# Performance work log

Hardware: AMD Instinct MI355X
Metric: run time of the kernel (lower is better)

## Reference

```python
import jax, jax.numpy as jnp
import numpy as np

N_NODES = 50000
N_EDGES = 800000
NFEAT, NHID, NCLASS = 512, 256, 64


def spmm(src, dst, w, h):
    """Sparse adj @ dense h via gather + segment_sum.
    out[i] = sum over edges e with dst[e]==i of w[e] * h[src[e]]."""
    msgs = h[src] * w[:, None]  # [E, d]
    return jax.ops.segment_sum(msgs, dst, num_segments=N_NODES)


def setup_inputs() -> dict:
    key = jax.random.key(0)
    ks = jax.random.split(key, 10)
    return {
        "x": jax.random.normal(ks[0], (N_NODES, NFEAT), dtype=jnp.float32),
        "edge_src0": jax.random.randint(ks[1], (N_EDGES,), 0, N_NODES),
        "edge_dst0": jax.random.randint(ks[2], (N_EDGES,), 0, N_NODES),
        "edge_w0": jax.random.uniform(ks[3], (N_EDGES,), dtype=jnp.float32),
        "edge_src1": jax.random.randint(ks[4], (N_EDGES,), 0, N_NODES),
        "edge_dst1": jax.random.randint(ks[5], (N_EDGES,), 0, N_NODES),
        "edge_w1": jax.random.uniform(ks[6], (N_EDGES,), dtype=jnp.float32),
        "W1": jax.random.normal(ks[7], (NFEAT, NHID), dtype=jnp.float32) * (1.0 / np.sqrt(NFEAT)),
        "b1": jnp.zeros((NHID,), dtype=jnp.float32),
        "W2": jax.random.normal(ks[8], (NHID, NCLASS), dtype=jnp.float32) * (1.0 / np.sqrt(NHID)),
        "b2": jnp.zeros((NCLASS,), dtype=jnp.float32),
    }


def reference(x, edge_src0, edge_dst0, edge_w0, edge_src1, edge_dst1, edge_w1, W1, b1, W2, b2):
    # Layer 1: GCN conv (skip=False) + ReLU. Dropout is identity in eval mode.
    h = jax.nn.relu(spmm(edge_src0, edge_dst0, edge_w0, x @ W1) + b1)
    # Layer 2: GCN conv (skip=False)
    logits = spmm(edge_src1, edge_dst1, edge_w1, h @ W2) + b2
    return jax.nn.log_softmax(logits, axis=1)
```

## Files before the change

kernel.cpp:

```cpp
#include <hip/hip_runtime.h>

#define N_NODES 50000
#define N_EDGES 800000
#define NFEAT   512
#define NHID    256
#define NCLASS  64

#define MTILES     ((N_NODES + 63) / 64)

#define NBUCK      196
#define BCAP       5632
#define BIN_CHUNK  4096
#define BIN_BLOCKS ((N_EDGES + BIN_CHUNK - 1) / BIN_CHUNK)

typedef short short8  __attribute__((ext_vector_type(8)));
typedef float floatx4 __attribute__((ext_vector_type(4)));
typedef float floatx2 __attribute__((ext_vector_type(2)));

__device__ inline short f2bf(float f) {
    unsigned u = __builtin_bit_cast(unsigned, f);
    u += 0x7FFF + ((u >> 16) & 1);
    return (short)(u >> 16);
}
__device__ inline float bf2f(short v) {
    unsigned u = ((unsigned)(unsigned short)v) << 16;
    return __builtin_bit_cast(float, u);
}
__device__ inline int pack_edge(int src, float w) {
    return (src & 0xFFFF) | ((int)(unsigned short)f2bf(w) << 16);
}

#if defined(__has_builtin)
#if __has_builtin(__builtin_amdgcn_cvt_pk_f32_fp8) && __has_builtin(__builtin_amdgcn_cvt_pk_fp8_f32)
#define HAVE_HW_FP8 1
#endif
#endif

__device__ inline unsigned char f2fp8(float f) {
#ifdef HAVE_HW_FP8
    return (unsigned char)(__builtin_amdgcn_cvt_pk_fp8_f32(f, f, 0, false) & 0xFF);
#else
    unsigned u = __builtin_bit_cast(unsigned, f);
    unsigned s = (u >> 31) << 7;
    float af = fabsf(f);
    if (!(af >= 0.0009765625f)) {
        int q = (int)(af * 512.f + 0.5f);
        if (q > 7) q = 7;
        return (unsigned char)(s | q);
    }
    if (af > 448.f) return (unsigned char)(s | 0x7E);
    int ex; float mf = frexpf(af, &ex);
    int E = ex - 1;
    if (E < -6) {
        int q = (int)(af * 512.f + 0.5f);
        if (q > 7) q = 7;
        return (unsigned char)(s | q);
    }
    int m = (int)((2.f * mf - 1.f) * 8.f + 0.5f);
    if (m == 8) { m = 0; ++E; }
    if (E > 8) return (unsigned char)(s | 0x7E);
    return (unsigned char)(s | ((E + 7) << 3) | m);
#endif
}

__device__ inline void fp8x8_to_f32(uint2 v, float* o) {
#ifdef HAVE_HW_FP8
    floatx2 f0 = __builtin_amdgcn_cvt_pk_f32_fp8((int)v.x, false);
    floatx2 f1 = __builtin_amdgcn_cvt_pk_f32_fp8((int)v.x, true);
    floatx2 f2 = __builtin_amdgcn_cvt_pk_f32_fp8((int)v.y, false);
    floatx2 f3 = __builtin_amdgcn_cvt_pk_f32_fp8((int)v.y, true);
    o[0] = f0[0]; o[1] = f0[1]; o[2] = f1[0]; o[3] = f1[1];
    o[4] = f2[0]; o[5] = f2[1]; o[6] = f3[0]; o[7] = f3[1];
#else
    unsigned w[2] = {v.x, v.y};
    #pragma unroll
    for (int k = 0; k < 8; ++k) {
        unsigned char b = (w[k >> 2] >> ((k & 3) * 8)) & 0xFF;
        int sg = b >> 7, e = (b >> 3) & 15, m = b & 7;
        float val = e ? ldexpf(1.f + m * 0.125f, e - 7) : ldexpf(m * 0.125f, -6);
        o[k] = sg ? -val : val;
    }
#endif
}

typedef __attribute__((address_space(3))) void       lds_void;
typedef __attribute__((address_space(1))) const void glb_void;
__device__ inline void gload_lds16(const void* g, void* l) {
    __builtin_amdgcn_global_load_lds((glb_void*)g, (lds_void*)l, 16, 0, 0);
}

__global__ __launch_bounds__(256) void cast_w1t_kernel(const float* __restrict__ W1,
                                                       short* __restrict__ Wt) {
    __shared__ short tile[64][72];
    const int t  = threadIdx.x;
    const int k0 = (blockIdx.x >> 2) << 6;
    const int n0 = (blockIdx.x & 3) << 6;
    {
        int kr = t >> 2, ng = (t & 3) << 4;
        const float* src = W1 + (size_t)(k0 + kr) * NHID + n0 + ng;
        float4 v0 = ((const float4*)src)[0], v1 = ((const float4*)src)[1];
        float4 v2 = ((const float4*)src)[2], v3 = ((const float4*)src)[3];
        short* d = &tile[kr][ng];
        d[0]=f2bf(v0.x); d[1]=f2bf(v0.y); d[2]=f2bf(v0.z); d[3]=f2bf(v0.w);
        d[4]=f2bf(v1.x); d[5]=f2bf(v1.y); d[6]=f2bf(v1.z); d[7]=f2bf(v1.w);
        d[8]=f2bf(v2.x); d[9]=f2bf(v2.y); d[10]=f2bf(v2.z); d[11]=f2bf(v2.w);
        d[12]=f2bf(v3.x); d[13]=f2bf(v3.y); d[14]=f2bf(v3.z); d[15]=f2bf(v3.w);
    }
    __syncthreads();
    {
        int nr = t >> 2, kg = (t & 3) << 4;
        short8 o0, o1;
        #pragma unroll
        for (int j = 0; j < 8; ++j) { o0[j] = tile[kg + j][nr]; o1[j] = tile[kg + 8 + j][nr]; }
        short* d = Wt + (size_t)(n0 + nr) * NFEAT + k0 + kg;
        *(short8*)d = o0;
        *(short8*)(d + 8) = o1;
    }
}

__global__ __launch_bounds__(256) void cast_w2t_kernel(const float* __restrict__ W2,
                                                       short* __restrict__ W2t) {
    __shared__ short tile[64][72];
    const int t  = threadIdx.x;
    const int k0 = blockIdx.x << 6;
    {
        int kr = t >> 2, ng = (t & 3) << 4;
        const float* src = W2 + (size_t)(k0 + kr) * NCLASS + ng;
        float4 v0 = ((const float4*)src)[0], v1 = ((const float4*)src)[1];
        float4 v2 = ((const float4*)src)[2], v3 = ((const float4*)src)[3];
        short* d = &tile[kr][ng];
        d[0]=f2bf(v0.x); d[1]=f2bf(v0.y); d[2]=f2bf(v0.z); d[3]=f2bf(v0.w);
        d[4]=f2bf(v1.x); d[5]=f2bf(v1.y); d[6]=f2bf(v1.z); d[7]=f2bf(v1.w);
        d[8]=f2bf(v2.x); d[9]=f2bf(v2.y); d[10]=f2bf(v2.z); d[11]=f2bf(v2.w);
        d[12]=f2bf(v3.x); d[13]=f2bf(v3.y); d[14]=f2bf(v3.z); d[15]=f2bf(v3.w);
    }
    __syncthreads();
    {
        int nr = t >> 2, kg = (t & 3) << 4;
        short8 o0, o1;
        #pragma unroll
        for (int j = 0; j < 8; ++j) { o0[j] = tile[kg + j][nr]; o1[j] = tile[kg + 8 + j][nr]; }
        short* d = W2t + (size_t)nr * NHID + k0 + kg;
        *(short8*)d = o0;
        *(short8*)(d + 8) = o1;
    }
}

__global__ __launch_bounds__(256) void binscatter_kernel(
    const int* __restrict__ es0, const int* __restrict__ ed0, const float* __restrict__ ew0,
    int* __restrict__ cur0, int2* __restrict__ bin0,
    const int* __restrict__ es1, const int* __restrict__ ed1, const float* __restrict__ ew1,
    int* __restrict__ cur1, int2* __restrict__ bin1) {
    __shared__ int hist[NBUCK];
    const int list = blockIdx.x >= BIN_BLOCKS;
    const int cb   = blockIdx.x - list * BIN_BLOCKS;
    const int*   es  = list ? es1 : es0;
    const int*   ed  = list ? ed1 : ed0;
    const float* ew  = list ? ew1 : ew0;
    int*         cur = list ? cur1 : cur0;
    int2*        bin = list ? bin1 : bin0;

    const int e0 = cb * BIN_CHUNK;
    const int e1 = min(e0 + BIN_CHUNK, N_EDGES);
    const int t  = threadIdx.x;

    if (t < NBUCK) hist[t] = 0;
    __syncthreads();
    for (int e = e0 + t; e < e1; e += 256)
        atomicAdd(&hist[ed[e] >> 8], 1);
    __syncthreads();
    if (t < NBUCK) hist[t] = atomicAdd(&cur[t], hist[t]);
    __syncthreads();
    for (int e = e0 + t; e < e1; e += 256) {
        int d = ed[e];
        int b = d >> 8;
        int p = atomicAdd(&hist[b], 1);
        if (p < BCAP) {
            int2 v; v.x = pack_edge(es[e], ew[e]); v.y = d;
            bin[(size_t)b * BCAP + p] = v;
        }
    }
}

__global__ __launch_bounds__(256) void bucket_scan_kernel(const int* __restrict__ cur0, int* __restrict__ bb0,
                                                          const int* __restrict__ cur1, int* __restrict__ bb1) {
    __shared__ int s[256];
    const int* cur = blockIdx.x ? cur1 : cur0;
    int*       bb  = blockIdx.x ? bb1  : bb0;
    int t = threadIdx.x;
    int v = (t < NBUCK) ? min(cur[t], BCAP) : 0;
    s[t] = v;
    __syncthreads();
    for (int off = 1; off < 256; off <<= 1) {
        int a = (t >= off) ? s[t - off] : 0;
        __syncthreads();
        s[t] += a;
        __syncthreads();
    }
    if (t < NBUCK) bb[t] = s[t] - v;
}

__global__ __launch_bounds__(256) void bucket_csr_kernel(
    const int* __restrict__ cur0, const int* __restrict__ bb0, const int2* __restrict__ bin0,
    int* __restrict__ deg0, int* __restrict__ base0, int* __restrict__ edge0,
    const int* __restrict__ cur1, const int* __restrict__ bb1, const int2* __restrict__ bin1,
    int* __restrict__ deg1, int* __restrict__ base1, int* __restrict__ edge1) {
    __shared__ int dh[256];
    __shared__ int sc[256];
    const int list = blockIdx.x >= NBUCK;
    const int b    = blockIdx.x - list * NBUCK;
    const int*  cur  = list ? cur1  : cur0;
    const int*  bb   = list ? bb1   : bb0;
    const int2* bin  = (list ? bin1 : bin0) + (size_t)b * BCAP;
    int*        deg  = list ? deg1  : deg0;
    int*        base = list ? base1 : base0;
    int*        edge = list ? edge1 : edge0;

    const int len   = min(cur[b], BCAP);
    const int gbase = bb[b];
    const int n0    = b << 8;
    const int t     = threadIdx.x;

    dh[t] = 0;
    __syncthreads();
    for (int i = t; i < len; i += 256)
        atomicAdd(&dh[bin[i].y & 255], 1);
    __syncthreads();
    int v = dh[t];
    sc[t] = v;
    __syncthreads();
    for (int off = 1; off < 256; off <<= 1) {
        int a = (t >= off) ? sc[t - off] : 0;
        __syncthreads();
        sc[t] += a;
        __syncthreads();
    }
    int excl = sc[t] - v;
    int node = n0 + t;
    if (node < N_NODES) { deg[node] = v; base[node] = gbase + excl; }
    dh[t] = gbase + excl;
    __syncthreads();
    for (int i = t; i < len; i += 256) {
        int2 ev = bin[i];
        int p = atomicAdd(&dh[ev.y & 255], 1);
        edge[p] = ev.x;
    }
}

__global__ __launch_bounds__(256) void gemm1_mfma_kernel(const float* __restrict__ x,
                                                         const short* __restrict__ Wt,
                                                         unsigned char* __restrict__ h0f) {
    __shared__ short As[64 * 64];
    __shared__ short Bs[256 * 64];
    const int tid  = threadIdx.x;
    const int wave = tid >> 6, lane = tid & 63;
    const int mlo  = lane & 15, q = lane >> 4;
    const int m0   = blockIdx.x * 64;

    const int ar = tid >> 2;
    const int cp = (tid & 3) * 2;
    int arow = m0 + ar; if (arow >= N_NODES) arow = N_NODES - 1;
    const float* aptr = x + (size_t)arow * NFEAT + cp * 8;

    const int brl = lane >> 3;
    const int bsl = lane & 7;

    floatx4 acc[4][4] = {};

    for (int kc = 0; kc < NFEAT; kc += 64) {
        #pragma unroll
        for (int i = 0; i < 8; ++i) {
            int r  = wave * 64 + i * 8 + brl;
            int sc2 = bsl ^ (r & 7);
            gload_lds16(Wt + (size_t)r * NFEAT + kc + sc2 * 8,
                        &Bs[(wave * 64 + i * 8) * 64]);
        }
        float4 a0 = *(const float4*)(aptr + kc);
        float4 a1 = *(const float4*)(aptr + kc + 4);
        float4 a2 = *(const float4*)(aptr + kc + 8);
        float4 a3 = *(const float4*)(aptr + kc + 12);
        short8 p0, p1;
        p0[0]=f2bf(a0.x); p0[1]=f2bf(a0.y); p0[2]=f2bf(a0.z); p0[3]=f2bf(a0.w);
        p0[4]=f2bf(a1.x); p0[5]=f2bf(a1.y); p0[6]=f2bf(a1.z); p0[7]=f2bf(a1.w);
        p1[0]=f2bf(a2.x); p1[1]=f2bf(a2.y); p1[2]=f2bf(a2.z); p1[3]=f2bf(a2.w);
        p1[4]=f2bf(a3.x); p1[5]=f2bf(a3.y); p1[6]=f2bf(a3.z); p1[7]=f2bf(a3.w);
        *(short8*)&As[ar * 64 + ((cp     ) ^ (ar & 7)) * 8] = p0;
        *(short8*)&As[ar * 64 + ((cp + 1) ^ (ar & 7)) * 8] = p1;
        __syncthreads();

        #pragma unroll
        for (int h = 0; h < 2; ++h) {
            short8 afv[4], bfv[4];
            #pragma unroll
            for (int t = 0; t < 4; ++t) {
                int r = t * 16 + mlo;
                afv[t] = *(const short8*)&As[r * 64 + ((h * 4 + q) ^ (r & 7)) * 8];
            }
            #pragma unroll
            for (int u = 0; u < 4; ++u) {
                int r = wave * 64 + u * 16 + mlo;
                bfv[u] = *(const short8*)&Bs[r * 64 + ((h * 4 + q) ^ (r & 7)) * 8];
            }
            #pragma unroll
            for (int t = 0; t < 4; ++t)
                #pragma unroll
                for (int u = 0; u < 4; ++u)
                    acc[t][u] = __builtin_amdgcn_mfma_f32_16x16x32_bf16(afv[t], bfv[u], acc[t][u], 0, 0, 0);
        }
        __syncthreads();
    }

    #pragma unroll
    for (int t = 0; t < 4; ++t) {
        #pragma unroll
        for (int r = 0; r < 4; ++r) {
            int row = m0 + t * 16 + q * 4 + r;
            if (row < N_NODES) {
                #pragma unroll
                for (int u = 0; u < 4; ++u)
                    h0f[(size_t)row * NHID + wave * 64 + u * 16 + mlo] = f2fp8(acc[t][u][r]);
            }
        }
    }
}

__global__ __launch_bounds__(256) void spmm1_pull_kernel(const int* __restrict__ base,
                                                         const int* __restrict__ deg,
                                                         const int* __restrict__ edge_s,
                                                         const unsigned char* __restrict__ h0f,
                                                         short* __restrict__ agg0b) {
    const int node = blockIdx.x * 4 + (threadIdx.x >> 6);
    const int lane = threadIdx.x & 63;
    const int slot = lane >> 5;
    const int c    = lane & 31;
    const int start = base[node];
    const int len   = deg[node];

    float acc[8] = {0.f,0.f,0.f,0.f,0.f,0.f,0.f,0.f};

    int eA = 0, eB = 0, eC = 0, eD = 0;
    uint2 z = {0u, 0u};
    uint2 hA = z, hB = z, hC = z;
    if (slot     < len) eA = edge_s[start + slot];
    if (slot + 2 < len) eB = edge_s[start + slot + 2];
    if (slot + 4 < len) eC = edge_s[start + slot + 4];
    if (slot + 6 < len) eD = edge_s[start + slot + 6];
    if (slot     < len) hA = *(const uint2*)(h0f + (size_t)(eA & 0xFFFF) * NHID + c * 8);
    if (slot + 2 < len) hB = *(const uint2*)(h0f + (size_t)(eB & 0xFFFF) * NHID + c * 8);
    if (slot + 4 < len) hC = *(const uint2*)(h0f + (size_t)(eC & 0xFFFF) * NHID + c * 8);

    int jr = slot + 6;
    int je = slot + 8;
    for (int j = slot; j < len; j += 2) {
        float wt = bf2f((short)((unsigned)eA >> 16));
        float f[8];
        fp8x8_to_f32(hA, f);
        #pragma unroll
        for (int k = 0; k < 8; ++k) acc[k] += wt * f[k];
        eA = eB; hA = hB;
        eB = eC; hB = hC;
        eC = eD;
        if (jr < len) hC = *(const uint2*)(h0f + (size_t)(eC & 0xFFFF) * NHID + c * 8);
        if (je < len) eD = edge_s[start + je];
        jr += 2; je += 2;
    }

    #pragma unroll
    for (int k = 0; k < 8; ++k) acc[k] += __shfl_xor(acc[k], 32);
    if (slot == 0) {
        short8 ob;
        #pragma unroll
        for (int k = 0; k < 8; ++k) ob[k] = f2bf(acc[k]);
        *(short8*)(agg0b + (size_t)node * NHID + c * 8) = ob;
    }
}

__global__ __launch_bounds__(256) void gemm2_mfma_kernel(const short* __restrict__ agg0b,
                                                         const float* __restrict__ b1,
                                                         const short* __restrict__ W2t,
                                                         short* __restrict__ h2b) {
    __shared__ short Bs[64 * 256];
    __shared__ short As[64 * 64];
    const int tid  = threadIdx.x;
    const int wave = tid >> 6, lane = tid & 63;
    const int mlo  = lane & 15, q = lane >> 4;
    const int m0   = blockIdx.x * 64;

    {
        int n = tid >> 2;
        #pragma unroll
        for (int j = 0; j < 8; ++j) {
            int c  = (tid & 3) * 8 + j;
            int s2 = c ^ (n & 7);
            *(short8*)&Bs[n * 256 + s2 * 8] =
                *(const short8*)(W2t + (size_t)n * NHID + c * 8);
        }
    }

    const int ar = tid >> 2;
    const int cp = (tid & 3) * 2;
    int arow = m0 + ar; if (arow >= N_NODES) arow = N_NODES - 1;
    const short* aptr = agg0b + (size_t)arow * NHID + cp * 8;

    floatx4 acc[4] = {};

    for (int kc = 0; kc < NHID; kc += 64) {
        short8 s0 = *(const short8*)(aptr + kc);
        short8 s1 = *(const short8*)(aptr + kc + 8);
        float4 c0 = *(const float4*)(b1 + kc + cp * 8);
        float4 c1 = *(const float4*)(b1 + kc + cp * 8 + 4);
        float4 c2 = *(const float4*)(b1 + kc + cp * 8 + 8);
        float4 c3 = *(const float4*)(b1 + kc + cp * 8 + 12);
        float v0 = bf2f(s0[0]) + c0.x, v1 = bf2f(s0[1]) + c0.y;
        float v2 = bf2f(s0[2]) + c0.z, v3 = bf2f(s0[3]) + c0.w;
        float v4 = bf2f(s0[4]) + c1.x, v5 = bf2f(s0[5]) + c1.y;
        float v6 = bf2f(s0[6]) + c1.z, v7 = bf2f(s0[7]) + c1.w;
        float v8 = bf2f(s1[0]) + c2.x, v9 = bf2f(s1[1]) + c2.y;
        float vA = bf2f(s1[2]) + c2.z, vB = bf2f(s1[3]) + c2.w;
        float vC = bf2f(s1[4]) + c3.x, vD = bf2f(s1[5]) + c3.y;
        float vE = bf2f(s1[6]) + c3.z, vF = bf2f(s1[7]) + c3.w;
        short8 p0, p1;
        p0[0]=f2bf(v0>0.f?v0:0.f); p0[1]=f2bf(v1>0.f?v1:0.f); p0[2]=f2bf(v2>0.f?v2:0.f); p0[3]=f2bf(v3>0.f?v3:0.f);
        p0[4]=f2bf(v4>0.f?v4:0.f); p0[5]=f2bf(v5>0.f?v5:0.f); p0[6]=f2bf(v6>0.f?v6:0.f); p0[7]=f2bf(v7>0.f?v7:0.f);
        p1[0]=f2bf(v8>0.f?v8:0.f); p1[1]=f2bf(v9>0.f?v9:0.f); p1[2]=f2bf(vA>0.f?vA:0.f); p1[3]=f2bf(vB>0.f?vB:0.f);
        p1[4]=f2bf(vC>0.f?vC:0.f); p1[5]=f2bf(vD>0.f?vD:0.f); p1[6]=f2bf(vE>0.f?vE:0.f); p1[7]=f2bf(vF>0.f?vF:0.f);
        *(short8*)&As[ar * 64 + ((cp     ) ^ (ar & 7)) * 8] = p0;
        *(short8*)&As[ar * 64 + ((cp + 1) ^ (ar & 7)) * 8] = p1;
        __syncthreads();

        short8 afv[2];
        {
            int r = wave * 16 + mlo;
            afv[0] = *(const short8*)&As[r * 64 + ((    q) ^ (r & 7)) * 8];
            afv[1] = *(const short8*)&As[r * 64 + ((4 + q) ^ (r & 7)) * 8];
        }
        #pragma unroll
        for (int u = 0; u < 4; ++u) {
            int r = u * 16 + mlo;
            #pragma unroll
            for (int h = 0; h < 2; ++h) {
                int ch = (kc >> 3) + h * 4 + q;
                short8 bv = *(const short8*)&Bs[r * 256 + (ch ^ (r & 7)) * 8];
                acc[u] = __builtin_amdgcn_mfma_f32_16x16x32_bf16(afv[h], bv, acc[u], 0, 0, 0);
            }
        }
        __syncthreads();
    }

    #pragma unroll
    for (int r = 0; r < 4; ++r) {
        int row = m0 + wave * 16 + q * 4 + r;
        if (row < N_NODES) {
            #pragma unroll
            for (int u = 0; u < 4; ++u)
                h2b[(size_t)row * NCLASS + u * 16 + mlo] = f2bf(acc[u][r]);
        }
    }
}

__global__ __launch_bounds__(256) void spmm2_lsm_kernel(const int* __restrict__ base,
                                                        const int* __restrict__ deg,
                                                        const int* __restrict__ edge_s,
                                                        const short* __restrict__ h2b,
                                                        const float* __restrict__ b2,
                                                        float* __restrict__ out) {
    const int node = blockIdx.x * 4 + (threadIdx.x >> 6);
    const int lane = threadIdx.x & 63;
    const int slot = lane >> 3;
    const int f    = lane & 7;
    const int start = base[node];
    const int len   = deg[node];

    float acc[8] = {0.f,0.f,0.f,0.f,0.f,0.f,0.f,0.f};
    int j = slot;
    int e = 0;
    short8 hv = {0,0,0,0,0,0,0,0};
    if (j < len) {
        e  = edge_s[start + j];
        hv = *(const short8*)(h2b + (size_t)(e & 0xFFFF) * NCLASS + f * 8);
    }
    while (j < len) {
        float wt = bf2f((short)((unsigned)e >> 16));
        int jn = j + 8;
        int en = e; short8 hn = hv;
        if (jn < len) {
            en = edge_s[start + jn];
            hn = *(const short8*)(h2b + (size_t)(en & 0xFFFF) * NCLASS + f * 8);
        }
        #pragma unroll
        for (int k = 0; k < 8; ++k) acc[k] += wt * bf2f(hv[k]);
        e = en; hv = hn; j = jn;
    }
    #pragma unroll
    for (int k = 0; k < 8; ++k) {
        acc[k] += __shfl_xor(acc[k], 8);
        acc[k] += __shfl_xor(acc[k], 16);
        acc[k] += __shfl_xor(acc[k], 32);
    }
    float4 c0 = *(const float4*)(b2 + f * 8);
    float4 c1 = *(const float4*)(b2 + f * 8 + 4);
    float v[8];
    v[0] = acc[0] + c0.x; v[1] = acc[1] + c0.y; v[2] = acc[2] + c0.z; v[3] = acc[3] + c0.w;
    v[4] = acc[4] + c1.x; v[5] = acc[5] + c1.y; v[6] = acc[6] + c1.z; v[7] = acc[7] + c1.w;
    float m = v[0];
    #pragma unroll
    for (int k = 1; k < 8; ++k) m = fmaxf(m, v[k]);
    m = fmaxf(m, __shfl_xor(m, 1));
    m = fmaxf(m, __shfl_xor(m, 2));
    m = fmaxf(m, __shfl_xor(m, 4));
    float s = 0.f;
    #pragma unroll
    for (int k = 0; k < 8; ++k) s += __expf(v[k] - m);
    s += __shfl_xor(s, 1);
    s += __shfl_xor(s, 2);
    s += __shfl_xor(s, 4);
    float ls = m + __logf(s);
    if (slot == 0) {
        float4 o0 = {v[0] - ls, v[1] - ls, v[2] - ls, v[3] - ls};
        float4 o1 = {v[4] - ls, v[5] - ls, v[6] - ls, v[7] - ls};
        float* p = out + (size_t)node * NCLASS + f * 8;
        *(float4*)p = o0;
        *(float4*)(p + 4) = o1;
    }
}

extern "C" void kernel_launch(void* const* d_in, const int* in_sizes, int n_in,
                              void* d_out, int out_size, void* d_ws, size_t ws_size,
                              hipStream_t stream) {
    const float* x   = (const float*)d_in[0];
    const int*   es0 = (const int*)  d_in[1];
    const int*   ed0 = (const int*)  d_in[2];
    const float* ew0 = (const float*)d_in[3];
    const int*   es1 = (const int*)  d_in[4];
    const int*   ed1 = (const int*)  d_in[5];
    const float* ew1 = (const float*)d_in[6];
    const float* W1  = (const float*)d_in[7];
    const float* b1  = (const float*)d_in[8];
    const float* W2  = (const float*)d_in[9];
    const float* b2  = (const float*)d_in[10];
    float* out = (float*)d_out;

    char* ws = (char*)d_ws;
    const size_t SZ_H0 = (size_t)N_NODES * NHID * sizeof(short);
    const size_t SZ_BIN = (size_t)NBUCK * BCAP * sizeof(int2);
    unsigned char* h0f = (unsigned char*)ws;
    short* h2b   = (short*)ws;
    short* agg0b = (short*)(ws + (size_t)N_NODES * NHID * sizeof(float));

    int2* bin0 = (int2*)(ws + SZ_H0);
    int2* bin1 = (int2*)(ws + SZ_H0 + SZ_BIN);

    char* c1 = ws + 44000000;
    int* deg1  = (int*)c1;
    int* base1 = deg1 + N_NODES;
    int* edge1 = base1 + N_NODES;
    int* cur0  = edge1 + N_EDGES;
    int* cur1  = cur0 + 256;
    int* bb0   = cur1 + 256;
    int* bb1   = bb0 + 256;

    int*   deg0  = (int*)d_out;
    int*   base0 = deg0 + N_NODES;
    int*   edge0 = base0 + N_NODES;
    short* Wt    = (short*)((char*)d_out + (8u << 20));
    short* W2t   = (short*)((char*)d_out + (9u << 20));

    hipMemsetAsync(cur0, 0, 512 * sizeof(int), stream);
    binscatter_kernel<<<2 * BIN_BLOCKS, 256, 0, stream>>>(es0, ed0, ew0, cur0, bin0,
                                                          es1, ed1, ew1, cur1, bin1);
    bucket_scan_kernel<<<2, 256, 0, stream>>>(cur0, bb0, cur1, bb1);
    bucket_csr_kernel<<<2 * NBUCK, 256, 0, stream>>>(cur0, bb0, bin0, deg0, base0, edge0,
                                                     cur1, bb1, bin1, deg1, base1, edge1);

    cast_w1t_kernel<<<32, 256, 0, stream>>>(W1, Wt);
    cast_w2t_kernel<<<4, 256, 0, stream>>>(W2, W2t);

    gemm1_mfma_kernel<<<MTILES, 256, 0, stream>>>(x, Wt, h0f);
    spmm1_pull_kernel<<<N_NODES / 4, 256, 0, stream>>>(base0, deg0, edge0, h0f, agg0b);

    gemm2_mfma_kernel<<<MTILES, 256, 0, stream>>>(agg0b, b1, W2t, h2b);
    spmm2_lsm_kernel<<<N_NODES / 4, 256, 0, stream>>>(base1, deg1, edge1, h2b, b2, out);
}
```

Baseline: 328.8 us.

## Merge prep kernels, fold bucket scan into CSR, double-buffer GEMM1, split SpMM1 features

Fuses edge binning and the two weight-transpose casts into one prep kernel, and folds the bucket prefix scan into the per-bucket CSR kernel, cutting the launch count. The first GEMM gets double-buffered LDS so the next K-chunk loads overlap the MFMA work, at the cost of twice the shared memory. The first SpMM now splits each node's 256 features across two blocks with four edge slots per wave instead of two, adding parallelism and memory-level concurrency. The cost is redundant edge-list reads and an extra shuffle reduction.

```diff
diff --git a/kernel.cpp b/kernel.cpp
--- a/kernel.cpp
+++ b/kernel.cpp
@@ -12,6 +12,7 @@
 #define BCAP       5632
 #define BIN_CHUNK  4096
 #define BIN_BLOCKS ((N_EDGES + BIN_CHUNK - 1) / BIN_CHUNK)
+#define PREP_BLOCKS (2 * BIN_BLOCKS + 32 + 4)
 
 typedef short short8  __attribute__((ext_vector_type(8)));
 typedef float floatx4 __attribute__((ext_vector_type(4)));
@@ -89,140 +90,131 @@
     __builtin_amdgcn_global_load_lds((glb_void*)g, (lds_void*)l, 16, 0, 0);
 }
 
-__global__ __launch_bounds__(256) void cast_w1t_kernel(const float* __restrict__ W1,
-                                                       short* __restrict__ Wt) {
-    __shared__ short tile[64][72];
-    const int t  = threadIdx.x;
-    const int k0 = (blockIdx.x >> 2) << 6;
-    const int n0 = (blockIdx.x & 3) << 6;
-    {
-        int kr = t >> 2, ng = (t & 3) << 4;
-        const float* src = W1 + (size_t)(k0 + kr) * NHID + n0 + ng;
-        float4 v0 = ((const float4*)src)[0], v1 = ((const float4*)src)[1];
-        float4 v2 = ((const float4*)src)[2], v3 = ((const float4*)src)[3];
-        short* d = &tile[kr][ng];
-        d[0]=f2bf(v0.x); d[1]=f2bf(v0.y); d[2]=f2bf(v0.z); d[3]=f2bf(v0.w);
-        d[4]=f2bf(v1.x); d[5]=f2bf(v1.y); d[6]=f2bf(v1.z); d[7]=f2bf(v1.w);
-        d[8]=f2bf(v2.x); d[9]=f2bf(v2.y); d[10]=f2bf(v2.z); d[11]=f2bf(v2.w);
-        d[12]=f2bf(v3.x); d[13]=f2bf(v3.y); d[14]=f2bf(v3.z); d[15]=f2bf(v3.w);
-    }
-    __syncthreads();
-    {
-        int nr = t >> 2, kg = (t & 3) << 4;
-        short8 o0, o1;
-        #pragma unroll
-        for (int j = 0; j < 8; ++j) { o0[j] = tile[kg + j][nr]; o1[j] = tile[kg + 8 + j][nr]; }
-        short* d = Wt + (size_t)(n0 + nr) * NFEAT + k0 + kg;
-        *(short8*)d = o0;
-        *(short8*)(d + 8) = o1;
-    }
-}
-
-__global__ __launch_bounds__(256) void cast_w2t_kernel(const float* __restrict__ W2,
-                                                       short* __restrict__ W2t) {
-    __shared__ short tile[64][72];
-    const int t  = threadIdx.x;
-    const int k0 = blockIdx.x << 6;
-    {
-        int kr = t >> 2, ng = (t & 3) << 4;
-        const float* src = W2 + (size_t)(k0 + kr) * NCLASS + ng;
-        float4 v0 = ((const float4*)src)[0], v1 = ((const float4*)src)[1];
-        float4 v2 = ((const float4*)src)[2], v3 = ((const float4*)src)[3];
-        short* d = &tile[kr][ng];
-        d[0]=f2bf(v0.x); d[1]=f2bf(v0.y); d[2]=f2bf(v0.z); d[3]=f2bf(v0.w);
-        d[4]=f2bf(v1.x); d[5]=f2bf(v1.y); d[6]=f2bf(v1.z); d[7]=f2bf(v1.w);
-        d[8]=f2bf(v2.x); d[9]=f2bf(v2.y); d[10]=f2bf(v2.z); d[11]=f2bf(v2.w);
-        d[12]=f2bf(v3.x); d[13]=f2bf(v3.y); d[14]=f2bf(v3.z); d[15]=f2bf(v3.w);
-    }
-    __syncthreads();
-    {
-        int nr = t >> 2, kg = (t & 3) << 4;
-        short8 o0, o1;
-        #pragma unroll
-        for (int j = 0; j < 8; ++j) { o0[j] = tile[kg + j][nr]; o1[j] = tile[kg + 8 + j][nr]; }
-        short* d = W2t + (size_t)nr * NHID + k0 + kg;
-        *(short8*)d = o0;
-        *(short8*)(d + 8) = o1;
-    }
-}
-
-__global__ __launch_bounds__(256) void binscatter_kernel(
+__global__ __launch_bounds__(256) void prep_kernel(
     const int* __restrict__ es0, const int* __restrict__ ed0, const float* __restrict__ ew0,
     int* __restrict__ cur0, int2* __restrict__ bin0,
     const int* __restrict__ es1, const int* __restrict__ ed1, const float* __restrict__ ew1,
-    int* __restrict__ cur1, int2* __restrict__ bin1) {
-    __shared__ int hist[NBUCK];
-    const int list = blockIdx.x >= BIN_BLOCKS;
-    const int cb   = blockIdx.x - list * BIN_BLOCKS;
-    const int*   es  = list ? es1 : es0;
-    const int*   ed  = list ? ed1 : ed0;
-    const float* ew  = list ? ew1 : ew0;
-    int*         cur = list ? cur1 : cur0;
-    int2*        bin = list ? bin1 : bin0;
-
-    const int e0 = cb * BIN_CHUNK;
-    const int e1 = min(e0 + BIN_CHUNK, N_EDGES);
-    const int t  = threadIdx.x;
-
-    if (t < NBUCK) hist[t] = 0;
-    __syncthreads();
-    for (int e = e0 + t; e < e1; e += 256)
-        atomicAdd(&hist[ed[e] >> 8], 1);
-    __syncthreads();
-    if (t < NBUCK) hist[t] = atomicAdd(&cur[t], hist[t]);
-    __syncthreads();
-    for (int e = e0 + t; e < e1; e += 256) {
-        int d = ed[e];
-        int b = d >> 8;
-        int p = atomicAdd(&hist[b], 1);
-        if (p < BCAP) {
-            int2 v; v.x = pack_edge(es[e], ew[e]); v.y = d;
-            bin[(size_t)b * BCAP + p] = v;
-        }
-    }
-}
-
-__global__ __launch_bounds__(256) void bucket_scan_kernel(const int* __restrict__ cur0, int* __restrict__ bb0,
-                                                          const int* __restrict__ cur1, int* __restrict__ bb1) {
-    __shared__ int s[256];
-    const int* cur = blockIdx.x ? cur1 : cur0;
-    int*       bb  = blockIdx.x ? bb1  : bb0;
-    int t = threadIdx.x;
-    int v = (t < NBUCK) ? min(cur[t], BCAP) : 0;
-    s[t] = v;
-    __syncthreads();
-    for (int off = 1; off < 256; off <<= 1) {
-        int a = (t >= off) ? s[t - off] : 0;
-        __syncthreads();
-        s[t] += a;
-        __syncthreads();
-    }
-    if (t < NBUCK) bb[t] = s[t] - v;
+    int* __restrict__ cur1, int2* __restrict__ bin1,
+    const float* __restrict__ W1, short* __restrict__ Wt,
+    const float* __restrict__ W2, short* __restrict__ W2t) {
+    __shared__ union {
+        int   hist[NBUCK];
+        short tile[64][72];
+    } sm;
+    const int blk = blockIdx.x;
+    const int t   = threadIdx.x;
+
+    if (blk < 2 * BIN_BLOCKS) {
+        const int list = blk >= BIN_BLOCKS;
+        const int cb   = blk - list * BIN_BLOCKS;
+        const int*   es  = list ? es1 : es0;
+        const int*   ed  = list ? ed1 : ed0;
+        const float* ew  = list ? ew1 : ew0;
+        int*         cur = list ? cur1 : cur0;
+        int2*        bin = list ? bin1 : bin0;
+
+        const int e0 = cb * BIN_CHUNK;
+        const int e1 = min(e0 + BIN_CHUNK, N_EDGES);
+
+        if (t < NBUCK) sm.hist[t] = 0;
+        __syncthreads();
+        for (int e = e0 + t; e < e1; e += 256)
+            atomicAdd(&sm.hist[ed[e] >> 8], 1);
+        __syncthreads();
+        if (t < NBUCK) sm.hist[t] = atomicAdd(&cur[t], sm.hist[t]);
+        __syncthreads();
+        for (int e = e0 + t; e < e1; e += 256) {
+            int d = ed[e];
+            int b = d >> 8;
+            int p = atomicAdd(&sm.hist[b], 1);
+            if (p < BCAP) {
+                int2 v; v.x = pack_edge(es[e], ew[e]); v.y = d;
+                bin[(size_t)b * BCAP + p] = v;
+            }
+        }
+    } else if (blk < 2 * BIN_BLOCKS + 32) {
+        const int cb = blk - 2 * BIN_BLOCKS;
+        const int k0 = (cb >> 2) << 6;
+        const int n0 = (cb & 3) << 6;
+        {
+            int kr = t >> 2, ng = (t & 3) << 4;
+            const float* src = W1 + (size_t)(k0 + kr) * NHID + n0 + ng;
+            float4 v0 = ((const float4*)src)[0], v1 = ((const float4*)src)[1];
+            float4 v2 = ((const float4*)src)[2], v3 = ((const float4*)src)[3];
+            short* d = &sm.tile[kr][ng];
+            d[0]=f2bf(v0.x); d[1]=f2bf(v0.y); d[2]=f2bf(v0.z); d[3]=f2bf(v0.w);
+            d[4]=f2bf(v1.x); d[5]=f2bf(v1.y); d[6]=f2bf(v1.z); d[7]=f2bf(v1.w);
+            d[8]=f2bf(v2.x); d[9]=f2bf(v2.y); d[10]=f2bf(v2.z); d[11]=f2bf(v2.w);
+            d[12]=f2bf(v3.x); d[13]=f2bf(v3.y); d[14]=f2bf(v3.z); d[15]=f2bf(v3.w);
+        }
+        __syncthreads();
+        {
+            int nr = t >> 2, kg = (t & 3) << 4;
+            short8 o0, o1;
+            #pragma unroll
+            for (int j = 0; j < 8; ++j) { o0[j] = sm.tile[kg + j][nr]; o1[j] = sm.tile[kg + 8 + j][nr]; }
+            short* d = Wt + (size_t)(n0 + nr) * NFEAT + k0 + kg;
+            *(short8*)d = o0;
+            *(short8*)(d + 8) = o1;
+        }
+    } else {
+        const int cb = blk - 2 * BIN_BLOCKS - 32;
+        const int k0 = cb << 6;
+        {
+            int kr = t >> 2, ng = (t & 3) << 4;
+            const float* src = W2 + (size_t)(k0 + kr) * NCLASS + ng;
+            float4 v0 = ((const float4*)src)[0], v1 = ((const float4*)src)[1];
+            float4 v2 = ((const float4*)src)[2], v3 = ((const float4*)src)[3];
+            short* d = &sm.tile[kr][ng];
+            d[0]=f2bf(v0.x); d[1]=f2bf(v0.y); d[2]=f2bf(v0.z); d[3]=f2bf(v0.w);
+            d[4]=f2bf(v1.x); d[5]=f2bf(v1.y); d[6]=f2bf(v1.z); d[7]=f2bf(v1.w);
+            d[8]=f2bf(v2.x); d[9]=f2bf(v2.y); d[10]=f2bf(v2.z); d[11]=f2bf(v2.w);
+            d[12]=f2bf(v3.x); d[13]=f2bf(v3.y); d[14]=f2bf(v3.z); d[15]=f2bf(v3.w);
+        }
+        __syncthreads();
+        {
+            int nr = t >> 2, kg = (t & 3) << 4;
+            short8 o0, o1;
+            #pragma unroll
+            for (int j = 0; j < 8; ++j) { o0[j] = sm.tile[kg + j][nr]; o1[j] = sm.tile[kg + 8 + j][nr]; }
+            short* d = W2t + (size_t)nr * NHID + k0 + kg;
+            *(short8*)d = o0;
+            *(short8*)(d + 8) = o1;
+        }
+    }
 }
 
 __global__ __launch_bounds__(256) void bucket_csr_kernel(
-    const int* __restrict__ cur0, const int* __restrict__ bb0, const int2* __restrict__ bin0,
+    const int* __restrict__ cur0, const int2* __restrict__ bin0,
     int* __restrict__ deg0, int* __restrict__ base0, int* __restrict__ edge0,
-    const int* __restrict__ cur1, const int* __restrict__ bb1, const int2* __restrict__ bin1,
+    const int* __restrict__ cur1, const int2* __restrict__ bin1,
     int* __restrict__ deg1, int* __restrict__ base1, int* __restrict__ edge1) {
     __shared__ int dh[256];
     __shared__ int sc[256];
+    __shared__ int pc[256];
     const int list = blockIdx.x >= NBUCK;
     const int b    = blockIdx.x - list * NBUCK;
     const int*  cur  = list ? cur1  : cur0;
-    const int*  bb   = list ? bb1   : bb0;
     const int2* bin  = (list ? bin1 : bin0) + (size_t)b * BCAP;
     int*        deg  = list ? deg1  : deg0;
     int*        base = list ? base1 : base0;
     int*        edge = list ? edge1 : edge0;
 
-    const int len   = min(cur[b], BCAP);
-    const int gbase = bb[b];
-    const int n0    = b << 8;
-    const int t     = threadIdx.x;
-
+    const int t = threadIdx.x;
+
+    pc[t] = (t < NBUCK) ? min(cur[t], BCAP) : 0;
     dh[t] = 0;
     __syncthreads();
+    for (int off = 1; off < 256; off <<= 1) {
+        int a = (t >= off) ? pc[t - off] : 0;
+        __syncthreads();
+        pc[t] += a;
+        __syncthreads();
+    }
+    const int gbase = b ? pc[b - 1] : 0;
+    const int len   = min(cur[b], BCAP);
+    const int n0    = b << 8;
+
     for (int i = t; i < len; i += 256)
         atomicAdd(&dh[bin[i].y & 255], 1);
     __syncthreads();
@@ -250,8 +242,8 @@
 __global__ __launch_bounds__(256) void gemm1_mfma_kernel(const float* __restrict__ x,
                                                          const short* __restrict__ Wt,
                                                          unsigned char* __restrict__ h0f) {
-    __shared__ short As[64 * 64];
-    __shared__ short Bs[256 * 64];
+    __shared__ short As[2][64 * 64];
+    __shared__ short Bs[2][256 * 64];
     const int tid  = threadIdx.x;
     const int wave = tid >> 6, lane = tid & 63;
     const int mlo  = lane & 15, q = lane >> 4;
@@ -267,58 +259,85 @@
 
     floatx4 acc[4][4] = {};
 
-    for (int kc = 0; kc < NFEAT; kc += 64) {
-        #pragma unroll
-        for (int i = 0; i < 8; ++i) {
-            int r  = wave * 64 + i * 8 + brl;
-            int sc2 = bsl ^ (r & 7);
-            gload_lds16(Wt + (size_t)r * NFEAT + kc + sc2 * 8,
-                        &Bs[(wave * 64 + i * 8) * 64]);
-        }
-        float4 a0 = *(const float4*)(aptr + kc);
-        float4 a1 = *(const float4*)(aptr + kc + 4);
-        float4 a2 = *(const float4*)(aptr + kc + 8);
-        float4 a3 = *(const float4*)(aptr + kc + 12);
+    #pragma unroll
+    for (int i = 0; i < 8; ++i) {
+        int r  = wave * 64 + i * 8 + brl;
+        int s2 = bsl ^ (r & 7);
+        gload_lds16(Wt + (size_t)r * NFEAT + s2 * 8, &Bs[0][(wave * 64 + i * 8) * 64]);
+    }
+    {
+        float4 a0 = *(const float4*)(aptr);
+        float4 a1 = *(const float4*)(aptr + 4);
+        float4 a2 = *(const float4*)(aptr + 8);
+        float4 a3 = *(const float4*)(aptr + 12);
         short8 p0, p1;
         p0[0]=f2bf(a0.x); p0[1]=f2bf(a0.y); p0[2]=f2bf(a0.z); p0[3]=f2bf(a0.w);
         p0[4]=f2bf(a1.x); p0[5]=f2bf(a1.y); p0[6]=f2bf(a1.z); p0[7]=f2bf(a1.w);
         p1[0]=f2bf(a2.x); p1[1]=f2bf(a2.y); p1[2]=f2bf(a2.z); p1[3]=f2bf(a2.w);
         p1[4]=f2bf(a3.x); p1[5]=f2bf(a3.y); p1[6]=f2bf(a3.z); p1[7]=f2bf(a3.w);
-        *(short8*)&As[ar * 64 + ((cp     ) ^ (ar & 7)) * 8] = p0;
-        *(short8*)&As[ar * 64 + ((cp + 1) ^ (ar & 7)) * 8] = p1;
-        __syncthreads();
-
+        *(short8*)&As[0][ar * 64 + ((cp     ) ^ (ar & 7)) * 8] = p0;
+        *(short8*)&As[0][ar * 64 + ((cp + 1) ^ (ar & 7)) * 8] = p1;
+    }
+    __syncthreads();
+
+    int cur = 0;
+    for (int kc = 0; kc < NFEAT; kc += 64) {
+        const int nxt = kc + 64;
+        float4 a0, a1, a2, a3;
+        if (nxt < NFEAT) {
+            #pragma unroll
+            for (int i = 0; i < 8; ++i) {
+                int r  = wave * 64 + i * 8 + brl;
+                int s2 = bsl ^ (r & 7);
+                gload_lds16(Wt + (size_t)r * NFEAT + nxt + s2 * 8,
+                            &Bs[cur ^ 1][(wave * 64 + i * 8) * 64]);
+            }
+            a0 = *(const float4*)(aptr + nxt);
+            a1 = *(const float4*)(aptr + nxt + 4);
+            a2 = *(const float4*)(aptr + nxt + 8);
+            a3 = *(const float4*)(aptr + nxt + 12);
+        }
         #pragma unroll
         for (int h = 0; h < 2; ++h) {
             short8 afv[4], bfv[4];
             #pragma unroll
-            for (int t = 0; t < 4; ++t) {
-                int r = t * 16 + mlo;
-                afv[t] = *(const short8*)&As[r * 64 + ((h * 4 + q) ^ (r & 7)) * 8];
+            for (int t2 = 0; t2 < 4; ++t2) {
+                int r = t2 * 16 + mlo;
+                afv[t2] = *(const short8*)&As[cur][r * 64 + ((h * 4 + q) ^ (r & 7)) * 8];
             }
             #pragma unroll
             for (int u = 0; u < 4; ++u) {
                 int r = wave * 64 + u * 16 + mlo;
-                bfv[u] = *(const short8*)&Bs[r * 64 + ((h * 4 + q) ^ (r & 7)) * 8];
+                bfv[u] = *(const short8*)&Bs[cur][r * 64 + ((h * 4 + q) ^ (r & 7)) * 8];
             }
             #pragma unroll
-            for (int t = 0; t < 4; ++t)
+            for (int t2 = 0; t2 < 4; ++t2)
                 #pragma unroll
                 for (int u = 0; u < 4; ++u)
-                    acc[t][u] = __builtin_amdgcn_mfma_f32_16x16x32_bf16(afv[t], bfv[u], acc[t][u], 0, 0, 0);
-        }
-        __syncthreads();
-    }
-
-    #pragma unroll
-    for (int t = 0; t < 4; ++t) {
+                    acc[t2][u] = __builtin_amdgcn_mfma_f32_16x16x32_bf16(afv[t2], bfv[u], acc[t2][u], 0, 0, 0);
+        }
+        if (nxt < NFEAT) {
+            short8 p0, p1;
+            p0[0]=f2bf(a0.x); p0[1]=f2bf(a0.y); p0[2]=f2bf(a0.z); p0[3]=f2bf(a0.w);
+            p0[4]=f2bf(a1.x); p0[5]=f2bf(a1.y); p0[6]=f2bf(a1.z); p0[7]=f2bf(a1.w);
+            p1[0]=f2bf(a2.x); p1[1]=f2bf(a2.y); p1[2]=f2bf(a2.z); p1[3]=f2bf(a2.w);
+            p1[4]=f2bf(a3.x); p1[5]=f2bf(a3.y); p1[6]=f2bf(a3.z); p1[7]=f2bf(a3.w);
+            *(short8*)&As[cur ^ 1][ar * 64 + ((cp     ) ^ (ar & 7)) * 8] = p0;
+            *(short8*)&As[cur ^ 1][ar * 64 + ((cp + 1) ^ (ar & 7)) * 8] = p1;
+        }
+        __syncthreads();
+        cur ^= 1;
+    }
+
+    #pragma unroll
+    for (int t2 = 0; t2 < 4; ++t2) {
         #pragma unroll
         for (int r = 0; r < 4; ++r) {
-            int row = m0 + t * 16 + q * 4 + r;
+            int row = m0 + t2 * 16 + q * 4 + r;
             if (row < N_NODES) {
                 #pragma unroll
                 for (int u = 0; u < 4; ++u)
-                    h0f[(size_t)row * NHID + wave * 64 + u * 16 + mlo] = f2fp8(acc[t][u][r]);
+                    h0f[(size_t)row * NHID + wave * 64 + u * 16 + mlo] = f2fp8(acc[t2][u][r]);
             }
         }
     }
@@ -329,10 +348,15 @@
                                                          const int* __restrict__ edge_s,
                                                          const unsigned char* __restrict__ h0f,
                                                          short* __restrict__ agg0b) {
-    const int node = blockIdx.x * 4 + (threadIdx.x >> 6);
+    const int g    = blockIdx.x;
+    const int r7   = g & 7;
+    const int half = r7 >> 2;
+    const int nb   = (g >> 3) * 4 + (r7 & 3);
+    const int node = nb * 4 + (threadIdx.x >> 6);
     const int lane = threadIdx.x & 63;
-    const int slot = lane >> 5;
-    const int c    = lane & 31;
+    const int slot = lane >> 4;
+    const int c    = lane & 15;
+    const int fof  = half * 128 + c * 8;
     const int start = base[node];
     const int len   = deg[node];
 
@@ -341,17 +365,17 @@
     int eA = 0, eB = 0, eC = 0, eD = 0;
     uint2 z = {0u, 0u};
     uint2 hA = z, hB = z, hC = z;
-    if (slot     < len) eA = edge_s[start + slot];
-    if (slot + 2 < len) eB = edge_s[start + slot + 2];
-    if (slot + 4 < len) eC = edge_s[start + slot + 4];
-    if (slot + 6 < len) eD = edge_s[start + slot + 6];
-    if (slot     < len) hA = *(const uint2*)(h0f + (size_t)(eA & 0xFFFF) * NHID + c * 8);
-    if (slot + 2 < len) hB = *(const uint2*)(h0f + (size_t)(eB & 0xFFFF) * NHID + c * 8);
-    if (slot + 4 < len) hC = *(const uint2*)(h0f + (size_t)(eC & 0xFFFF) * NHID + c * 8);
-
-    int jr = slot + 6;
-    int je = slot + 8;
-    for (int j = slot; j < len; j += 2) {
+    if (slot      < len) eA = edge_s[start + slot];
+    if (slot + 4  < len) eB = edge_s[start + slot + 4];
+    if (slot + 8  < len) eC = edge_s[start + slot + 8];
+    if (slot + 12 < len) eD = edge_s[start + slot + 12];
+    if (slot      < len) hA = *(const uint2*)(h0f + (size_t)(eA & 0xFFFF) * NHID + fof);
+    if (slot + 4  < len) hB = *(const uint2*)(h0f + (size_t)(eB & 0xFFFF) * NHID + fof);
+    if (slot + 8  < len) hC = *(const uint2*)(h0f + (size_t)(eC & 0xFFFF) * NHID + fof);
+
+    int jr = slot + 12;
+    int je = slot + 16;
+    for (int j = slot; j < len; j += 4) {
         float wt = bf2f((short)((unsigned)eA >> 16));
         float f[8];
         fp8x8_to_f32(hA, f);
@@ -360,18 +384,21 @@
         eA = eB; hA = hB;
         eB = eC; hB = hC;
         eC = eD;
-        if (jr < len) hC = *(const uint2*)(h0f + (size_t)(eC & 0xFFFF) * NHID + c * 8);
+        if (jr < len) hC = *(const uint2*)(h0f + (size_t)(eC & 0xFFFF) * NHID + fof);
         if (je < len) eD = edge_s[start + je];
-        jr += 2; je += 2;
-    }
-
-    #pragma unroll
-    for (int k = 0; k < 8; ++k) acc[k] += __shfl_xor(acc[k], 32);
+        jr += 4; je += 4;
+    }
+
+    #pragma unroll
+    for (int k = 0; k < 8; ++k) {
+        acc[k] += __shfl_xor(acc[k], 16);
+        acc[k] += __shfl_xor(acc[k], 32);
+    }
     if (slot == 0) {
         short8 ob;
         #pragma unroll
         for (int k = 0; k < 8; ++k) ob[k] = f2bf(acc[k]);
-        *(short8*)(agg0b + (size_t)node * NHID + c * 8) = ob;
+        *(short8*)(agg0b + (size_t)node * NHID + fof) = ob;
     }
 }
 
@@ -556,8 +583,6 @@
     int* edge1 = base1 + N_NODES;
     int* cur0  = edge1 + N_EDGES;
     int* cur1  = cur0 + 256;
-    int* bb0   = cur1 + 256;
-    int* bb1   = bb0 + 256;
 
     int*   deg0  = (int*)d_out;
     int*   base0 = deg0 + N_NODES;
@@ -566,17 +591,14 @@
     short* W2t   = (short*)((char*)d_out + (9u << 20));
 
     hipMemsetAsync(cur0, 0, 512 * sizeof(int), stream);
-    binscatter_kernel<<<2 * BIN_BLOCKS, 256, 0, stream>>>(es0, ed0, ew0, cur0, bin0,
-                                                          es1, ed1, ew1, cur1, bin1);
-    bucket_scan_kernel<<<2, 256, 0, stream>>>(cur0, bb0, cur1, bb1);
-    bucket_csr_kernel<<<2 * NBUCK, 256, 0, stream>>>(cur0, bb0, bin0, deg0, base0, edge0,
-                                                     cur1, bb1, bin1, deg1, base1, edge1);
-
-    cast_w1t_kernel<<<32, 256, 0, stream>>>(W1, Wt);
-    cast_w2t_kernel<<<4, 256, 0, stream>>>(W2, W2t);
+    prep_kernel<<<PREP_BLOCKS, 256, 0, stream>>>(es0, ed0, ew0, cur0, bin0,
+                                                 es1, ed1, ew1, cur1, bin1,
+                                                 W1, Wt, W2, W2t);
+    bucket_csr_kernel<<<2 * NBUCK, 256, 0, stream>>>(cur0, bin0, deg0, base0, edge0,
+                                                     cur1, bin1, deg1, base1, edge1);
 
     gemm1_mfma_kernel<<<MTILES, 256, 0, stream>>>(x, Wt, h0f);
-    spmm1_pull_kernel<<<N_NODES / 4, 256, 0, stream>>>(base0, deg0, edge0, h0f, agg0b);
+    spmm1_pull_kernel<<<2 * (N_NODES / 4), 256, 0, stream>>>(base0, deg0, edge0, h0f, agg0b);
 
     gemm2_mfma_kernel<<<MTILES, 256, 0, stream>>>(agg0b, b1, W2t, h2b);
     spmm2_lsm_kernel<<<N_NODES / 4, 256, 0, stream>>>(base1, deg1, edge1, h2b, b2, out);
```

New measurement: 328.4 us. Within noise of the previous version (-0.1%).
